# Optimization experiments

Hardware: AMD Instinct MI355X
Metric: run time of the kernel (lower is better)

## Reference

```python
import jax, jax.numpy as jnp
import numpy as np

# ---- config (matches init_kwargs) ----
B = 4                 # batch_size
A = 262144            # anchors per example (1048576 total / 4)
PRE_NMS = 4000        # fpn_pre_nms_top_n
POST_NMS = 1000       # fpn_post_nms_top_n
NMS_THRESH = 0.3
AUG_THICK = 0.2       # nms_aug_thickness: minimum size used when computing IoU


def setup_inputs() -> dict:
    key = jax.random.key(0)
    k1, k2, k3, k4, k5 = jax.random.split(key, 5)
    N = B * A
    objectness = jax.random.normal(k1, (N,), dtype=jnp.float32)
    box_regression = 0.1 * jax.random.normal(k2, (N, 7), dtype=jnp.float32)
    # realistic anchors: centers in a 50m scene, sizes in [0.5, 4.0], yaw in [-pi, pi]
    centers = jax.random.uniform(k3, (N, 3), dtype=jnp.float32) * 50.0
    sizes = 0.5 + jax.random.uniform(k4, (N, 3), dtype=jnp.float32) * 3.5
    yaw = (jax.random.uniform(k5, (N, 1), dtype=jnp.float32) - 0.5) * (2.0 * np.pi)
    anchors = jnp.concatenate([centers, sizes, yaw], axis=-1)
    return {"objectness": objectness, "box_regression": box_regression, "anchors": anchors}


def _decode(reg, anc):
    # SECOND-style 3D box decode. anc/reg: [..., 7] = (x, y, z_bottom, sx, sy, sz, yaw)
    xa, ya, za, wa, la, ha, ra = [anc[..., i] for i in range(7)]
    dx, dy, dz, dw, dl, dh, dr = [reg[..., i] for i in range(7)]
    diag = jnp.sqrt(wa * wa + la * la)
    x = dx * diag + xa
    y = dy * diag + ya
    z = dz * ha + za
    w = jnp.exp(dw) * wa
    l = jnp.exp(dl) * la
    h = jnp.exp(dh) * ha
    r = dr + ra
    return jnp.stack([x, y, z, w, l, h, r], axis=-1)


def _iou3d_matrix(boxes, aug):
    # Axis-aligned 3D IoU with thickness augmentation (min size clamp).
    # boxes: [N, 7], 'yx_zb' mode -> z is the bottom of the box.
    x, y, z0 = boxes[:, 0], boxes[:, 1], boxes[:, 2]
    sx = jnp.maximum(boxes[:, 3], aug)
    sy = jnp.maximum(boxes[:, 4], aug)
    sz = jnp.maximum(boxes[:, 5], aug)
    lo = jnp.stack([x - sx / 2, y - sy / 2, z0], axis=-1)          # [N,3]
    hi = jnp.stack([x + sx / 2, y + sy / 2, z0 + sz], axis=-1)     # [N,3]
    inter_lo = jnp.maximum(lo[:, None, :], lo[None, :, :])         # [N,N,3]
    inter_hi = jnp.minimum(hi[:, None, :], hi[None, :, :])
    inter = jnp.prod(jnp.maximum(inter_hi - inter_lo, 0.0), axis=-1)  # [N,N]
    vol = sx * sy * sz
    union = vol[:, None] + vol[None, :] - inter
    return inter / jnp.maximum(union, 1e-8)


def _greedy_nms(iou, thresh):
    # boxes assumed sorted by descending score. Returns keep mask [N] (bool).
    n = iou.shape[0]
    idx = jnp.arange(n)

    def body(i, keep):
        cur = keep[i]
        suppress = (idx > i) & cur & (iou[i] > thresh)
        return keep & (~suppress)

    keep0 = jnp.ones((n,), dtype=bool)
    return jax.lax.fori_loop(0, n, body, keep0)


def _per_example(obj_logits, reg, anc):
    # obj_logits: [A], reg/anc: [A, 7]
    scores = jax.nn.sigmoid(obj_logits)
    top_scores, top_idx = jax.lax.top_k(scores, PRE_NMS)          # sorted desc
    boxes = _decode(reg[top_idx], anc[top_idx])                   # [PRE,7]
    iou = _iou3d_matrix(boxes, AUG_THICK)
    keep = _greedy_nms(iou, NMS_THRESH)
    # stable select: kept boxes first (score order preserved), take first POST_NMS
    rank_key = jnp.where(keep, 0, PRE_NMS) + jnp.arange(PRE_NMS)
    order = jnp.argsort(rank_key)
    sel = order[:POST_NMS]
    valid = keep[sel].astype(boxes.dtype)                         # [POST]
    out_boxes = boxes[sel] * valid[:, None]
    out_scores = top_scores[sel] * valid
    return jnp.concatenate([out_boxes, out_scores[:, None]], axis=-1)  # [POST,8]


def reference(objectness, box_regression, anchors):
    obj = objectness.reshape(B, A)
    reg = box_regression.reshape(B, A, 7)
    anc = anchors.reshape(B, A, 7)
    return jax.vmap(_per_example)(obj, reg, anc)                  # [B, POST, 8]
```

## Files before the change

### kernel.cpp

```cpp
#include <hip/hip_runtime.h>
#include <math.h>

typedef unsigned int u32;
typedef unsigned long long u64;

#define BB 4
#define AA 262144
#define NN (BB*AA)
#define PRE 4000
#define POST 1000
#define CAP 4096
#define CAPR 5632
#define MASKW 64
#define NBLK 63
#define NCHUNK 125
#define SLICES 64
#define RSLICE 8

static const size_t OFF_CNTG = 0;
static const size_t OFF_CNTE = 512;
static const size_t OFF_KEYS = 1024;
static const size_t OFF_RANK = OFF_KEYS + (size_t)BB*CAPR*8;
static const size_t ZERO_END = OFF_RANK + (size_t)BB*CAPR*4;
static const size_t OFF_HC   = ZERO_END;
static const size_t OFF_HF   = OFF_HC + 262144;
static const size_t OFF_CROW = OFF_HF + 262144 + 384;
static const size_t OFF_NBOX = OFF_CROW + (size_t)BB*CAP*8*4;
static const size_t OFF_MASK = OFF_NBOX + (size_t)BB*CAP*8*4;

__device__ __forceinline__ u32 sigmoid_bits(float x) {
  float e = (float)exp(-(double)x);
  float s = 1.0f / (1.0f + e);
  return __float_as_uint(s);
}

__device__ __forceinline__ u32 mono_bits(float x) {
  u32 f = __float_as_uint(x);
  return (f & 0x80000000u) ? ~f : (f | 0x80000000u);
}

__global__ __launch_bounds__(256) void k_hcoarse(const float* __restrict__ obj,
                                                 u32* __restrict__ hc,
                                                 u64* __restrict__ zws) {
  __shared__ u32 lh[256*16];
  int tid = threadIdx.x;
  for (int i = tid; i < 256*16; i += 256) lh[i] = 0;
  int zidx = blockIdx.x*256 + tid;
  if (zidx < (int)(ZERO_END/8)) zws[zidx] = 0;
  __syncthreads();
  size_t blockBase = (size_t)blockIdx.x * 4096;
  int rep = tid & 15;
  for (int k = 0; k < 16; ++k) {
    u32 tt = mono_bits(obj[blockBase + (size_t)k*256 + tid]);
    atomicAdd(&lh[(tt >> 24)*16 + rep], 1u);
  }
  __syncthreads();
  u32 s = 0;
  #pragma unroll
  for (int r = 0; r < 16; ++r) s += lh[tid*16 + r];
  hc[(size_t)blockIdx.x*256 + tid] = s;
}

__global__ __launch_bounds__(256) void k_hfine(const float* __restrict__ obj,
                                               const u32* __restrict__ hc,
                                               u32* __restrict__ hf) {
  __shared__ u32 sum[256];
  __shared__ u32 lh[256];
  __shared__ u32 Cs;
  int tid = threadIdx.x;
  size_t blockBase = (size_t)blockIdx.x * 4096;
  int b = (int)(blockBase >> 18);
  {
    const u32* basep = hc + (size_t)b*SLICES*256;
    u32 s = 0;
    for (int k = 0; k < SLICES; ++k) s += basep[k*256 + tid];
    sum[tid] = s;
  }
  lh[tid] = 0;
  __syncthreads();
  if (tid == 0) {
    u32 acc = 0; int cs = 0;
    for (int i = 255; i >= 0; --i) {
      u32 c = sum[i];
      if (acc + c >= (u32)PRE) { cs = i; break; }
      acc += c;
    }
    Cs = (u32)cs;
  }
  __syncthreads();
  u32 C = Cs;
  for (int k = 0; k < 16; ++k) {
    u32 tt = mono_bits(obj[blockBase + (size_t)k*256 + tid]);
    if ((tt >> 24) == C) atomicAdd(&lh[(tt >> 16) & 255u], 1u);
  }
  __syncthreads();
  hf[(size_t)blockIdx.x*256 + tid] = lh[tid];
}

__global__ __launch_bounds__(256) void k_compact(const float* __restrict__ obj,
                                                 const u32* __restrict__ hc,
                                                 const u32* __restrict__ hf,
                                                 int* __restrict__ cntG,
                                                 int* __restrict__ cntE,
                                                 u64* __restrict__ keys) {
  __shared__ u32 sum[256];
  __shared__ u64 st[2048];
  __shared__ int nG, nE, baseG, baseE;
  __shared__ u32 Cs, As, Ps;
  int tid = threadIdx.x;
  size_t blockBase = (size_t)blockIdx.x * 4096;
  int b = (int)(blockBase >> 18);
  {
    const u32* basep = hc + (size_t)b*SLICES*256;
    u32 s = 0;
    for (int k = 0; k < SLICES; ++k) s += basep[k*256 + tid];
    sum[tid] = s;
  }
  if (tid == 0) { nG = 0; nE = 0; }
  __syncthreads();
  if (tid == 0) {
    u32 acc = 0; int cs = 0;
    for (int i = 255; i >= 0; --i) {
      u32 c = sum[i];
      if (acc + c >= (u32)PRE) { cs = i; break; }
      acc += c;
    }
    Cs = (u32)cs; As = acc;
  }
  __syncthreads();
  {
    const u32* basep = hf + (size_t)b*SLICES*256;
    u32 s = 0;
    for (int k = 0; k < SLICES; ++k) s += basep[k*256 + tid];
    sum[tid] = s;
  }
  __syncthreads();
  if (tid == 0) {
    u32 acc = As; int fb = 0;
    for (int i = 255; i >= 0; --i) {
      u32 c = sum[i];
      if (acc + c >= (u32)PRE) { fb = i; break; }
      acc += c;
    }
    Ps = (Cs << 8) | (u32)fb;
  }
  __syncthreads();
  u32 P = Ps;
  for (int k = 0; k < 16; ++k) {
    size_t g = blockBase + (size_t)k*256 + tid;
    float x = obj[g];
    u32 tb = mono_bits(x) >> 16;
    if (tb + 1u >= P) {
      u32 m = sigmoid_bits(x);
      u64 key = ((u64)m << 32) | (u64)(AA - 1 - (u32)(g & (AA - 1)));
      if (tb > P) { int p = atomicAdd(&nG, 1); if (p < 1536) st[p] = key; }
      else        { int p = atomicAdd(&nE, 1); if (p < 512) st[2047 - p] = key; }
    }
  }
  __syncthreads();
  int ng = nG < 1536 ? nG : 1536;
  int ne = nE < 512 ? nE : 512;
  if (tid == 0) baseG = atomicAdd(&cntG[b*32], ng);
  if (tid == 1) baseE = atomicAdd(&cntE[b*32], ne);
  __syncthreads();
  for (int i = tid; i < ng; i += 256) {
    int p = baseG + i;
    if (p < 4000) keys[(size_t)b*CAPR + p] = st[i];
  }
  for (int i = tid; i < ne; i += 256) {
    int p = baseE + i;
    if (p < CAPR - 4000) keys[(size_t)b*CAPR + 4000 + p] = st[2047 - i];
  }
}

__global__ __launch_bounds__(64) void k_rankp(const u64* __restrict__ keys,
                                              u32* __restrict__ rank) {
  int b = blockIdx.z;
  int slot = blockIdx.x*64 + threadIdx.x;
  const u64* kb = keys + (size_t)b*CAPR;
  u64 myk = kb[slot];
  const ulonglong2* p2 = (const ulonglong2*)(kb + blockIdx.y*(CAPR/RSLICE));
  int r = 0;
  for (int base = 0; base < CAPR/(2*RSLICE); base += 16) {
    ulonglong2 v[16];
    #pragma unroll
    for (int k = 0; k < 16; ++k) v[k] = p2[base + k];
    #pragma unroll
    for (int k = 0; k < 16; ++k)
      r += (int)(v[k].x > myk) + (int)(v[k].y > myk);
  }
  if (r) atomicAdd(&rank[b*CAPR + slot], (u32)r);
}

__global__ __launch_bounds__(256) void k_decode(const u64* __restrict__ keys,
                                                const u32* __restrict__ rank,
                                                const float* __restrict__ reg,
                                                const float* __restrict__ anc,
                                                float* __restrict__ crow,
                                                float* __restrict__ nbox) {
  int t = blockIdx.x*256 + threadIdx.x;
  int b = t / CAPR, slot = t - b*CAPR;
  u64 myk = keys[(size_t)b*CAPR + slot];
  int rk = (int)rank[b*CAPR + slot];
  if (myk == 0 || rk >= PRE) return;
  u32 m = (u32)(myk >> 32);
  int idx = AA - 1 - (int)(myk & 0xFFFFFFFFull);
  float score = __uint_as_float(m);
  size_t g = ((size_t)b << 18) + (size_t)idx;
  const float* rg = reg + g*7;
  const float* an = anc + g*7;
  float xa=an[0], ya=an[1], za=an[2], wa=an[3], la=an[4], ha=an[5], ra=an[6];
  float dx=rg[0], dy=rg[1], dz=rg[2], dw=rg[3], dl=rg[4], dh=rg[5], dr=rg[6];
  float diag = sqrtf(wa*wa + la*la);
  float x = dx*diag + xa;
  float y = dy*diag + ya;
  float z = dz*ha + za;
  float w = expf(dw)*wa;
  float l = expf(dl)*la;
  float h = expf(dh)*ha;
  float r = dr + ra;
  float* cr = crow + ((size_t)b*CAP + rk)*8;
  cr[0]=x; cr[1]=y; cr[2]=z; cr[3]=w; cr[4]=l; cr[5]=h; cr[6]=r; cr[7]=score;
  float sx = fmaxf(w, 0.2f), sy = fmaxf(l, 0.2f), sz = fmaxf(h, 0.2f);
  float* nb = nbox + ((size_t)b*CAP + rk)*8;
  nb[0]=x - sx*0.5f; nb[1]=y - sy*0.5f; nb[2]=z;
  nb[3]=x + sx*0.5f; nb[4]=y + sy*0.5f; nb[5]=z + sz;
  nb[6]=sx*sy*sz;   nb[7]=0.f;
}

__global__ __launch_bounds__(256) void k_mask(const float* __restrict__ nbox,
                                              u64* __restrict__ mask) {
  int c = blockIdx.x;
  int R = blockIdx.y;
  int b = blockIdx.z;
  if (c < R*4) return;
  __shared__ float4 ca4[64], cb4[64];
  int t = threadIdx.x;
  int j0 = c*64;
  if (t < 64) {
    int j = j0 + t; int jc = j < PRE ? j : 0;
    const float4* p = (const float4*)(nbox + ((size_t)b*CAP + jc)*8);
    ca4[t] = p[0]; cb4[t] = p[1];
  }
  __syncthreads();
  int i = R*256 + t;
  if (i >= PRE) return;
  const float4* rp = (const float4*)(nbox + ((size_t)b*CAP + i)*8);
  float4 A = rp[0], Bv = rp[1];
  u64 bits = 0;
  #pragma unroll
  for (int jj = 0; jj < 64; ++jj) {
    float4 C = ca4[jj], D = cb4[jj];
    float d0 = fminf(A.w,  C.w) - fmaxf(A.x, C.x);
    float d1 = fminf(Bv.x, D.x) - fmaxf(A.y, C.y);
    float d2 = fminf(Bv.y, D.y) - fmaxf(A.z, C.z);
    float inter = fmaxf(d0, 0.f) * fmaxf(d1, 0.f) * fmaxf(d2, 0.f);
    float uni = Bv.z + D.z - inter;
    if (inter > 0.3f * uni) bits |= (1ull << jj);
  }
  int vcols = PRE - j0;
  if (vcols < 64) bits &= ((1ull << vcols) - 1ull);
  if (j0 <= i) {
    int d = i - j0;
    if (d >= 63) bits = 0;
    else bits &= ~((2ull << d) - 1ull);
  }
  mask[((size_t)b*MASKW + c)*PRE + i] = bits;
}

__device__ __forceinline__ void load_chunk(u64 (&buf)[32], const u64* col,
                                           int c, int lane) {
  bool act = lane >= (c >> 1);
  const ulonglong2* p = (const ulonglong2*)(col + c*32);
  #pragma unroll
  for (int k = 0; k < 16; ++k) {
    ulonglong2 v; v.x = 0; v.y = 0;
    if (act) v = p[k];
    buf[2*k] = v.x; buf[2*k+1] = v.y;
  }
}

__device__ __forceinline__ void resolve_chunk(u64 (&buf)[32], int c, int lane,
                                              u64& removed, int& kc,
                                              int* __restrict__ sel_lds) {
  int wq = c >> 1;
  int base = (c & 1) * 32;
  u64 cur = removed, km = 0;
  #pragma unroll
  for (int jj = 0; jj < 32; ++jj) {
    if (((cur >> (base + jj)) & 1ull) == 0ull) {
      km |= (1ull << (base + jj));
      cur |= buf[jj];
    }
  }
  u64 kmw = __shfl(km, wq, 64);
  #pragma unroll
  for (int jj = 0; jj < 32; ++jj) {
    if ((kmw >> (base + jj)) & 1ull) removed |= buf[jj];
  }
  int sh = base + (lane & 31);
  bool mine = (lane < 32) && ((kmw >> sh) & 1ull);
  int pos = kc + (int)__popcll(kmw & ((1ull << sh) - 1ull));
  if (mine && pos < POST) sel_lds[pos] = c*32 + lane;
  kc += (int)__popcll(kmw);
}

__global__ __launch_bounds__(64) void k_reduce(const u64* __restrict__ mask,
                                               const float* __restrict__ crow,
                                               float* __restrict__ out) {
  __shared__ int sel_lds[POST];
  int b = blockIdx.x, lane = threadIdx.x;
  const u64* col = mask + ((size_t)b*MASKW + lane)*PRE;
  u64 bufA[32], bufB[32];
  u64 removed = 0;
  int kc = 0;
  load_chunk(bufA, col, 0, lane);
  for (int c = 0; c < NCHUNK; c += 2) {
    if (c + 1 < NCHUNK) load_chunk(bufB, col, c + 1, lane);
    resolve_chunk(bufA, c, lane, removed, kc, sel_lds);
    if (kc >= POST) break;
    if (c + 1 >= NCHUNK) break;
    if (c + 2 < NCHUNK) load_chunk(bufA, col, c + 2, lane);
    resolve_chunk(bufB, c + 1, lane, removed, kc, sel_lds);
    if (kc >= POST) break;
  }
  __syncthreads();
  int kcap = kc < POST ? kc : POST;
  for (int r = lane; r < POST; r += 64) {
    float4 o0 = make_float4(0.f,0.f,0.f,0.f), o1 = o0;
    if (r < kcap) {
      int i = sel_lds[r];
      const float4* p = (const float4*)(crow + ((size_t)b*CAP + i)*8);
      o0 = p[0]; o1 = p[1];
    }
    float4* q = (float4*)(out + ((size_t)b*POST + r)*8);
    q[0] = o0; q[1] = o1;
  }
}

extern "C" void kernel_launch(void* const* d_in, const int* in_sizes, int n_in,
                              void* d_out, int out_size, void* d_ws, size_t ws_size,
                              hipStream_t stream) {
  const float* obj = (const float*)d_in[0];
  const float* reg = (const float*)d_in[1];
  const float* anc = (const float*)d_in[2];
  float* out = (float*)d_out;
  char* ws = (char*)d_ws;

  int*  cntG = (int*)(ws + OFF_CNTG);
  int*  cntE = (int*)(ws + OFF_CNTE);
  u64*  keys = (u64*)(ws + OFF_KEYS);
  u32*  rank = (u32*)(ws + OFF_RANK);
  u32*  hc   = (u32*)(ws + OFF_HC);
  u32*  hf   = (u32*)(ws + OFF_HF);
  float* crow = (float*)(ws + OFF_CROW);
  float* nbox = (float*)(ws + OFF_NBOX);
  u64*  mask = (u64*)(ws + OFF_MASK);

  k_hcoarse<<<NN/4096, 256, 0, stream>>>(obj, hc, (u64*)ws);
  k_hfine<<<NN/4096, 256, 0, stream>>>(obj, hc, hf);
  k_compact<<<NN/4096, 256, 0, stream>>>(obj, hc, hf, cntG, cntE, keys);
  k_rankp<<<dim3(CAPR/64, RSLICE, BB), 64, 0, stream>>>(keys, rank);
  k_decode<<<(BB*CAPR)/256, 256, 0, stream>>>(keys, rank, reg, anc, crow, nbox);
  k_mask<<<dim3(NBLK, 16, BB), 256, 0, stream>>>(nbox, mask);
  k_reduce<<<BB, 64, 0, stream>>>(mask, crow, out);
}
```

Measured before the change: 218.0 us.

## Split serial NMS reduce across 8 waves with LDS token passing

```diff
diff --git a/kernel.cpp b/kernel.cpp
--- a/kernel.cpp
+++ b/kernel.cpp
@@ -16,6 +16,8 @@
 #define NCHUNK 125
 #define SLICES 64
 #define RSLICE 8
+#define RWAVES 8
+#define STOPVAL 0x7fffffff
 
 static const size_t OFF_CNTG = 0;
 static const size_t OFF_CNTE = 512;
@@ -280,6 +282,13 @@
   }
 }
 
+__device__ __forceinline__ void force_loaded(u64 (&buf)[32]) {
+  u64 a = 0;
+  #pragma unroll
+  for (int j = 0; j < 32; ++j) a ^= buf[j];
+  asm volatile("" :: "v"(a));
+}
+
 __device__ __forceinline__ void resolve_chunk(u64 (&buf)[32], int c, int lane,
                                               u64& removed, int& kc,
                                               int* __restrict__ sel_lds) {
@@ -305,28 +314,71 @@
   kc += (int)__popcll(kmw);
 }
 
-__global__ __launch_bounds__(64) void k_reduce(const u64* __restrict__ mask,
-                                               const float* __restrict__ crow,
-                                               float* __restrict__ out) {
+__global__ __launch_bounds__(RWAVES*64, 1) void k_reduce(const u64* __restrict__ mask,
+                                                         const float* __restrict__ crow,
+                                                         float* __restrict__ out) {
+  __shared__ u64 rem_lds[64];
   __shared__ int sel_lds[POST];
-  int b = blockIdx.x, lane = threadIdx.x;
+  __shared__ int kc_lds;
+  __shared__ int flag;
+  int b = blockIdx.x;
+  int tid = threadIdx.x;
+  int w = tid >> 6;
+  int lane = tid & 63;
   const u64* col = mask + ((size_t)b*MASKW + lane)*PRE;
+  if (tid < 64) rem_lds[tid] = 0;
+  if (tid == 0) { kc_lds = 0; flag = 0; }
+  __syncthreads();
+
   u64 bufA[32], bufB[32];
-  u64 removed = 0;
-  int kc = 0;
-  load_chunk(bufA, col, 0, lane);
-  for (int c = 0; c < NCHUNK; c += 2) {
-    if (c + 1 < NCHUNK) load_chunk(bufB, col, c + 1, lane);
-    resolve_chunk(bufA, c, lane, removed, kc, sel_lds);
-    if (kc >= POST) break;
-    if (c + 1 >= NCHUNK) break;
-    if (c + 2 < NCHUNK) load_chunk(bufA, col, c + 2, lane);
-    resolve_chunk(bufB, c + 1, lane, removed, kc, sel_lds);
-    if (kc >= POST) break;
-  }
-  __syncthreads();
+  load_chunk(bufA, col, w, lane);
+  load_chunk(bufB, col, w + RWAVES, lane);
+  force_loaded(bufA);
+  force_loaded(bufB);
+
+  auto turn = [&](u64 (&buf)[32], int c) -> bool {
+    int v;
+    for (;;) {
+      v = __hip_atomic_load(&flag, __ATOMIC_ACQUIRE, __HIP_MEMORY_SCOPE_WORKGROUP);
+      if (v >= c) break;
+      __builtin_amdgcn_s_sleep(1);
+    }
+    if (v != c) return true;
+    asm volatile("s_waitcnt lgkmcnt(0)" ::: "memory");
+    u64 removed = rem_lds[lane];
+    int kc = kc_lds;
+    resolve_chunk(buf, c, lane, removed, kc, sel_lds);
+    rem_lds[lane] = removed;
+    if (lane == 0) kc_lds = kc;
+    __threadfence_block();
+    int nf = (kc >= POST || c + 1 >= NCHUNK) ? STOPVAL : c + 1;
+    __hip_atomic_store(&flag, nf, __ATOMIC_RELEASE, __HIP_MEMORY_SCOPE_WORKGROUP);
+    return nf == STOPVAL;
+  };
+
+  bool stop = false;
+  int c = w;
+  while (!stop) {
+    stop = turn(bufA, c);
+    if (!stop && c + 2*RWAVES < NCHUNK) {
+      load_chunk(bufA, col, c + 2*RWAVES, lane);
+      force_loaded(bufA);
+    }
+    c += RWAVES;
+    if (stop || c >= NCHUNK) break;
+    stop = turn(bufB, c);
+    if (!stop && c + 2*RWAVES < NCHUNK) {
+      load_chunk(bufB, col, c + 2*RWAVES, lane);
+      force_loaded(bufB);
+    }
+    c += RWAVES;
+    if (c >= NCHUNK) break;
+  }
+
+  __syncthreads();
+  int kc = kc_lds;
   int kcap = kc < POST ? kc : POST;
-  for (int r = lane; r < POST; r += 64) {
+  for (int r = tid; r < POST; r += RWAVES*64) {
     float4 o0 = make_float4(0.f,0.f,0.f,0.f), o1 = o0;
     if (r < kcap) {
       int i = sel_lds[r];
@@ -363,5 +415,5 @@
   k_rankp<<<dim3(CAPR/64, RSLICE, BB), 64, 0, stream>>>(keys, rank);
   k_decode<<<(BB*CAPR)/256, 256, 0, stream>>>(keys, rank, reg, anc, crow, nbox);
   k_mask<<<dim3(NBLK, 16, BB), 256, 0, stream>>>(nbox, mask);
-  k_reduce<<<BB, 64, 0, stream>>>(mask, crow, out);
-}
+  k_reduce<<<BB, RWAVES*64, 0, stream>>>(mask, crow, out);
+}
```

Result: slower. 224.6 us (+3.0%).
